# Performance work log

Measured on AMD Instinct MI355X. Metric: run time of the kernel, lower is better.

Reference implementation:

```python
import jax, jax.numpy as jnp
import numpy as np

IN_FEATURES = 512
OUT_FEATURES = 256
N = 2048

def setup_inputs() -> dict:
    key = jax.random.key(0)
    k1, k2, k3 = jax.random.split(key, 3)
    x = jax.random.normal(k1, (N, IN_FEATURES), dtype=jnp.float32)
    # kaiming_uniform_(a=sqrt(5)) -> uniform(-b, b) with b = sqrt(6/((1+5)*fan_in)) = 1/sqrt(fan_in)
    bound_w = 1.0 / np.sqrt(IN_FEATURES)
    weight = jax.random.uniform(k2, (OUT_FEATURES, IN_FEATURES), dtype=jnp.float32,
                                minval=-bound_w, maxval=bound_w)
    bound_b = 1.0 / np.sqrt(IN_FEATURES)
    bias = jax.random.uniform(k3, (OUT_FEATURES,), dtype=jnp.float32,
                              minval=-bound_b, maxval=bound_b)
    return {"x": x, "weight": weight, "bias": bias}

def reference(x, weight, bias):
    # MAM fully-connected (beta == 0 path):
    # prod[n, k, j] = x[n, k] * weight[j, k]
    # C[n, j] = max_k prod[n,k,j] + min_k prod[n,k,j] + bias[j]
    prod = x[:, :, None] * weight.T[None, :, :]   # [N, in, out]
    C = jnp.max(prod, axis=1) + jnp.min(prod, axis=1) + bias[None, :]
    return C
```

## Files before the change

kernel.cpp:

```cpp
#include <hip/hip_runtime.h>
#include <math.h>

#define NROWS 2048
#define INF_ 512
#define OUTF 256

__global__ __launch_bounds__(256) void mam_partial(
    const float* __restrict__ x, const float* __restrict__ w,
    float* __restrict__ pmax, float* __restrict__ pmin, int kLen)
{
    __shared__ __align__(16) float xs[32][68];
    __shared__ __align__(16) float wsh[32][68];

    const int t  = threadIdx.x;
    const int j0 = blockIdx.x * 64;
    const int n0 = blockIdx.y * 64;
    const int k0 = blockIdx.z * kLen;

    const int tx = t & 15;
    const int ty = t >> 4;

    float mx[4][4], mn[4][4];
#pragma unroll
    for (int i = 0; i < 4; ++i)
#pragma unroll
        for (int j = 0; j < 4; ++j) {
            mx[i][j] = -__builtin_inff();
            mn[i][j] =  __builtin_inff();
        }

    for (int c = 0; c < kLen; c += 32) {
        const int kc = k0 + c;
#pragma unroll
        for (int p = 0; p < 2; ++p) {
            int idx = t + p * 256;
            int n = idx >> 3, kv = idx & 7;
            float4 g = ((const float4*)(x + (size_t)(n0 + n) * INF_ + kc))[kv];
            xs[kv * 4 + 0][n] = g.x;
            xs[kv * 4 + 1][n] = g.y;
            xs[kv * 4 + 2][n] = g.z;
            xs[kv * 4 + 3][n] = g.w;
        }
#pragma unroll
        for (int p = 0; p < 2; ++p) {
            int idx = t + p * 256;
            int j = idx >> 3, kv = idx & 7;
            float4 g = ((const float4*)(w + (size_t)(j0 + j) * INF_ + kc))[kv];
            wsh[kv * 4 + 0][j] = g.x;
            wsh[kv * 4 + 1][j] = g.y;
            wsh[kv * 4 + 2][j] = g.z;
            wsh[kv * 4 + 3][j] = g.w;
        }
        __syncthreads();

#pragma unroll
        for (int kk = 0; kk < 32; ++kk) {
            float4 xv = *(const float4*)&xs[kk][ty * 4];
            float4 wv = *(const float4*)&wsh[kk][tx * 4];
            float xa[4] = {xv.x, xv.y, xv.z, xv.w};
            float wa[4] = {wv.x, wv.y, wv.z, wv.w};
#pragma unroll
            for (int i = 0; i < 4; ++i)
#pragma unroll
                for (int j = 0; j < 4; ++j) {
                    float p = xa[i] * wa[j];
                    mx[i][j] = fmaxf(mx[i][j], p);
                    mn[i][j] = fminf(mn[i][j], p);
                }
        }
        __syncthreads();
    }

    const size_t sOff = (size_t)blockIdx.z * NROWS * OUTF;
#pragma unroll
    for (int i = 0; i < 4; ++i) {
        size_t row = (size_t)(n0 + ty * 4 + i) * OUTF + j0 + tx * 4;
        float4 vmx = make_float4(mx[i][0], mx[i][1], mx[i][2], mx[i][3]);
        float4 vmn = make_float4(mn[i][0], mn[i][1], mn[i][2], mn[i][3]);
        *(float4*)(pmax + sOff + row) = vmx;
        *(float4*)(pmin + sOff + row) = vmn;
    }
}

__global__ __launch_bounds__(256) void mam_combine(
    const float* __restrict__ pmax, const float* __restrict__ pmin,
    const float* __restrict__ bias, float* __restrict__ out, int S)
{
    const int f = blockIdx.x * 256 + threadIdx.x;
    const int PLANE4 = NROWS * OUTF / 4;
    const float4* pm4 = (const float4*)pmax;
    const float4* pn4 = (const float4*)pmin;

    float4 a = pm4[f];
    float4 b = pn4[f];
    for (int s = 1; s < S; ++s) {
        float4 a2 = pm4[(size_t)s * PLANE4 + f];
        float4 b2 = pn4[(size_t)s * PLANE4 + f];
        a.x = fmaxf(a.x, a2.x); a.y = fmaxf(a.y, a2.y);
        a.z = fmaxf(a.z, a2.z); a.w = fmaxf(a.w, a2.w);
        b.x = fminf(b.x, b2.x); b.y = fminf(b.y, b2.y);
        b.z = fminf(b.z, b2.z); b.w = fminf(b.w, b2.w);
    }
    float4 bi = ((const float4*)bias)[f & 63];
    float4 o;
    o.x = a.x + b.x + bi.x;
    o.y = a.y + b.y + bi.y;
    o.z = a.z + b.z + bi.z;
    o.w = a.w + b.w + bi.w;
    ((float4*)out)[f] = o;
}

__global__ __launch_bounds__(256) void mam_naive(
    const float* __restrict__ x, const float* __restrict__ w,
    const float* __restrict__ bias, float* __restrict__ out)
{
    const int n = blockIdx.x;
    const int j = threadIdx.x;
    float mx = -__builtin_inff(), mn = __builtin_inff();
    for (int k = 0; k < INF_; ++k) {
        float p = x[(size_t)n * INF_ + k] * w[(size_t)j * INF_ + k];
        mx = fmaxf(mx, p);
        mn = fminf(mn, p);
    }
    out[(size_t)n * OUTF + j] = mx + mn + bias[j];
}

extern "C" void kernel_launch(void* const* d_in, const int* in_sizes, int n_in,
                              void* d_out, int out_size, void* d_ws, size_t ws_size,
                              hipStream_t stream) {
    const float* x    = (const float*)d_in[0];
    const float* w    = (const float*)d_in[1];
    const float* bias = (const float*)d_in[2];
    float* out = (float*)d_out;

    const size_t plane = (size_t)NROWS * OUTF * sizeof(float);
    int S;
    if      (ws_size >= 8 * plane) S = 4;
    else if (ws_size >= 4 * plane) S = 2;
    else if (ws_size >= 2 * plane) S = 1;
    else                           S = 0;

    if (S > 0) {
        float* pmax = (float*)d_ws;
        float* pmin = pmax + (size_t)S * NROWS * OUTF;
        dim3 grid(OUTF / 64, NROWS / 64, S);
        mam_partial<<<grid, 256, 0, stream>>>(x, w, pmax, pmin, INF_ / S);
        mam_combine<<<(NROWS * OUTF / 4) / 256, 256, 0, stream>>>(pmax, pmin, bias, out, S);
    } else {
        mam_naive<<<NROWS, 256, 0, stream>>>(x, w, bias, out);
    }
}
```

Baseline: 87.33 us.

## Raise K-split to 8, single-stage swizzled smem tiles, packed multiplies

The K split is fixed at 8, so each block loads its whole 64-wide K slice of x and w into shared memory once, with a rotating float4 swizzle, and needs only one barrier. The inner loop reads float4 along K for both operands and does the products as packed 2-wide float multiplies. An occupancy hint of 4 blocks per CU is added, and the grid grows to 1024 blocks to improve CU fill. The cost is twice as much partial-result traffic through the combine kernel. The kernel also now needs 32MB of workspace, and if that is not available it falls back to the very slow naive kernel.

```diff
diff --git a/kernel.cpp b/kernel.cpp
--- a/kernel.cpp
+++ b/kernel.cpp
@@ -1,107 +1,104 @@
 #include <hip/hip_runtime.h>
 #include <math.h>
 
-#define NROWS 2048
-#define INF_ 512
-#define OUTF 256
+#define N_ 2048
+#define K_ 512
+#define J_ 256
+#define SPLIT 8
+#define KR  (K_ / SPLIT)
+#define KR4 (KR / 4)
 
-__global__ __launch_bounds__(256) void mam_partial(
+typedef __attribute__((ext_vector_type(2))) float v2f;
+
+__global__ __launch_bounds__(256, 4) void mam_partial(
     const float* __restrict__ x, const float* __restrict__ w,
-    float* __restrict__ pmax, float* __restrict__ pmin, int kLen)
+    float* __restrict__ pmax, float* __restrict__ pmin)
 {
-    __shared__ __align__(16) float xs[32][68];
-    __shared__ __align__(16) float wsh[32][68];
+    __shared__ __align__(16) float xs[64 * 64];
+    __shared__ __align__(16) float wsh[64 * 64];
 
     const int t  = threadIdx.x;
-    const int j0 = blockIdx.x * 64;
-    const int n0 = blockIdx.y * 64;
-    const int k0 = blockIdx.z * kLen;
-
     const int tx = t & 15;
     const int ty = t >> 4;
+    const int n0 = blockIdx.x * 64;
+    const int j0 = blockIdx.y * 64;
+    const int kc = blockIdx.z * KR;
+
+#pragma unroll
+    for (int r = 0; r < 4; ++r) {
+        const int idx = r * 256 + t;
+        const int row = idx >> 4;
+        const int kq  = idx & 15;
+        const int c   = (kq + (row >> 2)) & 15;
+        const float4 gx = *(const float4*)(x + (size_t)(n0 + row) * K_ + kc + kq * 4);
+        *(float4*)&xs[row * 64 + c * 4] = gx;
+        const float4 gw = *(const float4*)(w + (size_t)(j0 + row) * K_ + kc + kq * 4);
+        *(float4*)&wsh[row * 64 + c * 4] = gw;
+    }
+    __syncthreads();
 
     float mx[4][4], mn[4][4];
 #pragma unroll
     for (int i = 0; i < 4; ++i)
 #pragma unroll
-        for (int j = 0; j < 4; ++j) {
-            mx[i][j] = -__builtin_inff();
-            mn[i][j] =  __builtin_inff();
+        for (int j = 0; j < 4; ++j) { mx[i][j] = -__builtin_inff(); mn[i][j] = __builtin_inff(); }
+
+#pragma unroll 4
+    for (int k4 = 0; k4 < KR4; ++k4) {
+        float4 xv[4], wv[4];
+#pragma unroll
+        for (int i = 0; i < 4; ++i)
+            xv[i] = *(const float4*)&xs[(ty * 4 + i) * 64 + (((k4 + ty) & 15) * 4)];
+#pragma unroll
+        for (int j = 0; j < 4; ++j)
+            wv[j] = *(const float4*)&wsh[(tx * 4 + j) * 64 + (((k4 + tx) & 15) * 4)];
+#pragma unroll
+        for (int i = 0; i < 4; ++i) {
+            const v2f xa = {xv[i].x, xv[i].y};
+            const v2f xb = {xv[i].z, xv[i].w};
+#pragma unroll
+            for (int j = 0; j < 4; ++j) {
+                const v2f wa = {wv[j].x, wv[j].y};
+                const v2f wb = {wv[j].z, wv[j].w};
+                const v2f pA = xa * wa;
+                const v2f pB = xb * wb;
+                mx[i][j] = fmaxf(fmaxf(mx[i][j], pA.x), pA.y);
+                mn[i][j] = fminf(fminf(mn[i][j], pA.x), pA.y);
+                mx[i][j] = fmaxf(fmaxf(mx[i][j], pB.x), pB.y);
+                mn[i][j] = fminf(fminf(mn[i][j], pB.x), pB.y);
+            }
         }
-
-    for (int c = 0; c < kLen; c += 32) {
-        const int kc = k0 + c;
-#pragma unroll
-        for (int p = 0; p < 2; ++p) {
-            int idx = t + p * 256;
-            int n = idx >> 3, kv = idx & 7;
-            float4 g = ((const float4*)(x + (size_t)(n0 + n) * INF_ + kc))[kv];
-            xs[kv * 4 + 0][n] = g.x;
-            xs[kv * 4 + 1][n] = g.y;
-            xs[kv * 4 + 2][n] = g.z;
-            xs[kv * 4 + 3][n] = g.w;
-        }
-#pragma unroll
-        for (int p = 0; p < 2; ++p) {
-            int idx = t + p * 256;
-            int j = idx >> 3, kv = idx & 7;
-            float4 g = ((const float4*)(w + (size_t)(j0 + j) * INF_ + kc))[kv];
-            wsh[kv * 4 + 0][j] = g.x;
-            wsh[kv * 4 + 1][j] = g.y;
-            wsh[kv * 4 + 2][j] = g.z;
-            wsh[kv * 4 + 3][j] = g.w;
-        }
-        __syncthreads();
-
-#pragma unroll
-        for (int kk = 0; kk < 32; ++kk) {
-            float4 xv = *(const float4*)&xs[kk][ty * 4];
-            float4 wv = *(const float4*)&wsh[kk][tx * 4];
-            float xa[4] = {xv.x, xv.y, xv.z, xv.w};
-            float wa[4] = {wv.x, wv.y, wv.z, wv.w};
-#pragma unroll
-            for (int i = 0; i < 4; ++i)
-#pragma unroll
-                for (int j = 0; j < 4; ++j) {
-                    float p = xa[i] * wa[j];
-                    mx[i][j] = fmaxf(mx[i][j], p);
-                    mn[i][j] = fminf(mn[i][j], p);
-                }
-        }
-        __syncthreads();
     }
 
-    const size_t sOff = (size_t)blockIdx.z * NROWS * OUTF;
+    const size_t base = ((size_t)blockIdx.z * N_ + n0 + ty * 4) * J_ + j0 + tx * 4;
 #pragma unroll
     for (int i = 0; i < 4; ++i) {
-        size_t row = (size_t)(n0 + ty * 4 + i) * OUTF + j0 + tx * 4;
-        float4 vmx = make_float4(mx[i][0], mx[i][1], mx[i][2], mx[i][3]);
-        float4 vmn = make_float4(mn[i][0], mn[i][1], mn[i][2], mn[i][3]);
-        *(float4*)(pmax + sOff + row) = vmx;
-        *(float4*)(pmin + sOff + row) = vmn;
+        *(float4*)(pmax + base + (size_t)i * J_) = make_float4(mx[i][0], mx[i][1], mx[i][2], mx[i][3]);
+        *(float4*)(pmin + base + (size_t)i * J_) = make_float4(mn[i][0], mn[i][1], mn[i][2], mn[i][3]);
     }
 }
 
 __global__ __launch_bounds__(256) void mam_combine(
     const float* __restrict__ pmax, const float* __restrict__ pmin,
-    const float* __restrict__ bias, float* __restrict__ out, int S)
+    const float* __restrict__ bias, float* __restrict__ out)
 {
     const int f = blockIdx.x * 256 + threadIdx.x;
-    const int PLANE4 = NROWS * OUTF / 4;
-    const float4* pm4 = (const float4*)pmax;
-    const float4* pn4 = (const float4*)pmin;
+    const int PLANE4 = N_ * J_ / 4;
+    const float4* pm = (const float4*)pmax;
+    const float4* pn = (const float4*)pmin;
 
-    float4 a = pm4[f];
-    float4 b = pn4[f];
-    for (int s = 1; s < S; ++s) {
-        float4 a2 = pm4[(size_t)s * PLANE4 + f];
-        float4 b2 = pn4[(size_t)s * PLANE4 + f];
+    float4 a = pm[f];
+    float4 b = pn[f];
+#pragma unroll
+    for (int s = 1; s < SPLIT; ++s) {
+        const float4 a2 = pm[(size_t)s * PLANE4 + f];
+        const float4 b2 = pn[(size_t)s * PLANE4 + f];
         a.x = fmaxf(a.x, a2.x); a.y = fmaxf(a.y, a2.y);
         a.z = fmaxf(a.z, a2.z); a.w = fmaxf(a.w, a2.w);
         b.x = fminf(b.x, b2.x); b.y = fminf(b.y, b2.y);
         b.z = fminf(b.z, b2.z); b.w = fminf(b.w, b2.w);
     }
-    float4 bi = ((const float4*)bias)[f & 63];
+    const float4 bi = ((const float4*)bias)[f & (J_ / 4 - 1)];
     float4 o;
     o.x = a.x + b.x + bi.x;
     o.y = a.y + b.y + bi.y;
@@ -117,12 +114,12 @@
     const int n = blockIdx.x;
     const int j = threadIdx.x;
     float mx = -__builtin_inff(), mn = __builtin_inff();
-    for (int k = 0; k < INF_; ++k) {
-        float p = x[(size_t)n * INF_ + k] * w[(size_t)j * INF_ + k];
+    for (int k = 0; k < K_; ++k) {
+        const float p = x[(size_t)n * K_ + k] * w[(size_t)j * K_ + k];
         mx = fmaxf(mx, p);
         mn = fminf(mn, p);
     }
-    out[(size_t)n * OUTF + j] = mx + mn + bias[j];
+    out[(size_t)n * J_ + j] = mx + mn + bias[j];
 }
 
 extern "C" void kernel_launch(void* const* d_in, const int* in_sizes, int n_in,
@@ -133,20 +130,14 @@
     const float* bias = (const float*)d_in[2];
     float* out = (float*)d_out;
 
-    const size_t plane = (size_t)NROWS * OUTF * sizeof(float);
-    int S;
-    if      (ws_size >= 8 * plane) S = 4;
-    else if (ws_size >= 4 * plane) S = 2;
-    else if (ws_size >= 2 * plane) S = 1;
-    else                           S = 0;
-
-    if (S > 0) {
+    const size_t need = (size_t)SPLIT * 2 * N_ * J_ * sizeof(float);
+    if (ws_size >= need) {
         float* pmax = (float*)d_ws;
-        float* pmin = pmax + (size_t)S * NROWS * OUTF;
-        dim3 grid(OUTF / 64, NROWS / 64, S);
-        mam_partial<<<grid, 256, 0, stream>>>(x, w, pmax, pmin, INF_ / S);
-        mam_combine<<<(NROWS * OUTF / 4) / 256, 256, 0, stream>>>(pmax, pmin, bias, out, S);
+        float* pmin = pmax + (size_t)SPLIT * N_ * J_;
+        dim3 grid(N_ / 64, J_ / 64, SPLIT);
+        mam_partial<<<grid, 256, 0, stream>>>(x, w, pmax, pmin);
+        mam_combine<<<(N_ * J_ / 4) / 256, 256, 0, stream>>>(pmax, pmin, bias, out);
     } else {
-        mam_naive<<<NROWS, 256, 0, stream>>>(x, w, bias, out);
+        mam_naive<<<N_, 256, 0, stream>>>(x, w, bias, out);
     }
 }
```

New measurement: 84.57 us. 1.03x faster.
